# Kernel tuning notes

Measured on AMD Instinct MI355X. Metric: run time of the kernel, lower is better.

Reference implementation:

```python
import jax, jax.numpy as jnp
import numpy as np
from functools import partial


def lstm(x, Wx, Wh, b, act):
    """Keras LSTM. x:[B,T,F]. Gate order i,f,c,o. Returns (all_h:[B,T,H], last_h:[B,H])."""
    B, T, _ = x.shape
    H = Wh.shape[0]
    xz = jnp.einsum('btf,fg->btg', x, Wx) + b  # precompute input projections
    def step(carry, xz_t):
        h, c = carry
        z = xz_t + h @ Wh
        i, f, g, o = jnp.split(z, 4, axis=-1)
        i = jax.nn.sigmoid(i); f = jax.nn.sigmoid(f)
        g = act(g); o = jax.nn.sigmoid(o)
        c = f * c + i * g
        h = o * act(c)
        return (h, c), h
    init = (jnp.zeros((B, H), x.dtype), jnp.zeros((B, H), x.dtype))
    (h_last, _), hs = jax.lax.scan(step, init, jnp.swapaxes(xz, 0, 1))
    return jnp.swapaxes(hs, 0, 1), h_last


def gru(x, Wx, Wh, b):
    """Keras GRU with reset_after=True. b:[2,3H]. Gate order z,r,h. Returns last h."""
    B, T, _ = x.shape
    H = Wh.shape[0]
    xz = jnp.einsum('btf,fg->btg', x, Wx) + b[0]
    def step(h, xz_t):
        rec = h @ Wh + b[1]
        xz_z, xz_r, xz_h = jnp.split(xz_t, 3, axis=-1)
        r_z, r_r, r_h = jnp.split(rec, 3, axis=-1)
        z = jax.nn.sigmoid(xz_z + r_z)
        r = jax.nn.sigmoid(xz_r + r_r)
        hh = jnp.tanh(xz_h + r * r_h)
        h = z * h + (1.0 - z) * hh
        return h, None
    h0 = jnp.zeros((B, H), x.dtype)
    h_last, _ = jax.lax.scan(step, h0, jnp.swapaxes(xz, 0, 1))
    return h_last


def setup_inputs() -> dict:
    key = jax.random.key(0)
    ks = jax.random.split(key, 32)
    s = 0.05  # small init so relu-LSTM stays numerically stable over 64 steps
    d = {}
    d['keypoint_data'] = jax.random.normal(ks[0], (256, 64, 1662), jnp.float32)
    d['img_data'] = jax.random.normal(ks[1], (256, 64, 2048), jnp.float32)
    # keypoint LSTM stack: 1662->64->128->64, gates=4H
    d['kW1x'] = s * jax.random.normal(ks[2], (1662, 256), jnp.float32)
    d['kW1h'] = s * jax.random.normal(ks[3], (64, 256), jnp.float32)
    d['kb1'] = jnp.zeros((256,), jnp.float32)
    d['kW2x'] = s * jax.random.normal(ks[4], (64, 512), jnp.float32)
    d['kW2h'] = s * jax.random.normal(ks[5], (128, 512), jnp.float32)
    d['kb2'] = jnp.zeros((512,), jnp.float32)
    d['kW3x'] = s * jax.random.normal(ks[6], (128, 256), jnp.float32)
    d['kW3h'] = s * jax.random.normal(ks[7], (64, 256), jnp.float32)
    d['kb3'] = jnp.zeros((256,), jnp.float32)
    # keypoint dense heads
    d['kD1w'] = s * jax.random.normal(ks[8], (64, 64), jnp.float32)
    d['kD1b'] = jnp.zeros((64,), jnp.float32)
    d['kD2w'] = s * jax.random.normal(ks[9], (64, 32), jnp.float32)
    d['kD2b'] = jnp.zeros((32,), jnp.float32)
    # img branch: LSTM 2048->64 (tanh), GRU 64->8 (reset_after bias [2,24])
    d['iWx'] = s * jax.random.normal(ks[10], (2048, 256), jnp.float32)
    d['iWh'] = s * jax.random.normal(ks[11], (64, 256), jnp.float32)
    d['ib'] = jnp.zeros((256,), jnp.float32)
    d['gWx'] = s * jax.random.normal(ks[12], (64, 24), jnp.float32)
    d['gWh'] = s * jax.random.normal(ks[13], (8, 24), jnp.float32)
    d['gb'] = jnp.zeros((2, 24), jnp.float32)
    d['iDw'] = s * jax.random.normal(ks[14], (8, 8), jnp.float32)
    d['iDb'] = jnp.zeros((8,), jnp.float32)
    # final dense on concat([img(8), key(32)]) -> num_classes
    d['fW'] = s * jax.random.normal(ks[15], (40, 10), jnp.float32)
    d['fb'] = jnp.zeros((10,), jnp.float32)
    return d


def reference(keypoint_data, img_data,
              kW1x, kW1h, kb1, kW2x, kW2h, kb2, kW3x, kW3h, kb3,
              kD1w, kD1b, kD2w, kD2b,
              iWx, iWh, ib, gWx, gWh, gb, iDw, iDb, fW, fb):
    relu = jax.nn.relu
    # keypoint branch: 3 relu-LSTMs
    h, _ = lstm(keypoint_data, kW1x, kW1h, kb1, relu)
    h, _ = lstm(h, kW2x, kW2h, kb2, relu)
    _, h = lstm(h, kW3x, kW3h, kb3, relu)  # return_sequences=False
    h = relu(h @ kD1w + kD1b)
    key_out = relu(h @ kD2w + kD2b)  # [B,32]
    # img branch: tanh LSTM -> GRU -> (dropout=identity at inference) -> dense
    hs, _ = lstm(img_data, iWx, iWh, ib, jnp.tanh)
    g = gru(hs, gWx, gWh, gb)  # [B,8]
    img_out = relu(g @ iDw + iDb)  # [B,8]
    combined = jnp.concatenate([img_out, key_out], axis=-1)  # [B,40]
    return jax.nn.softmax(combined @ fW + fb, axis=-1)
```

## Files before the change

### kernel.cpp

```cpp
#include <hip/hip_runtime.h>


typedef short bf16x8 __attribute__((ext_vector_type(8)));
typedef float f32x4 __attribute__((ext_vector_type(4)));

__device__ __forceinline__ unsigned f2bf(float x) {
    unsigned u = __float_as_uint(x);
    return (u + 0x7FFFu + ((u >> 16) & 1u)) >> 16;
}
__device__ __forceinline__ float bf2f(unsigned b) { return __uint_as_float(b << 16); }
__device__ __forceinline__ float sigmoidf_(float x) { return 1.f / (1.f + __expf(-x)); }
__device__ __forceinline__ float tanhf_(float x) {
    float e = __expf(2.f * x);
    return 1.f - 2.f / (e + 1.f);
}

__device__ __forceinline__ void cvt2(float x0, float x1, unsigned& hp, unsigned& lp) {
    unsigned h;
    asm("v_cvt_pk_bf16_f32 %0, %1, %2" : "=v"(h) : "v"(x0), "v"(x1));
    float a0 = __uint_as_float(h << 16);
    float a1 = __uint_as_float(h & 0xffff0000u);
    unsigned l;
    asm("v_cvt_pk_bf16_f32 %0, %1, %2" : "=v"(l) : "v"(x0 - a0), "v"(x1 - a1));
    hp = h; lp = l;
}

template<int K, int N>
__device__ __forceinline__ void split_w(const float* __restrict__ W,
                                        unsigned short* __restrict__ hi,
                                        unsigned short* __restrict__ lo, int item) {
    int kt = item / N;
    int n  = item % N;
    unsigned uh[16], ul[16];
#pragma unroll
    for (int p = 0; p < 16; p++) {
        unsigned h2[2], l2[2];
#pragma unroll
        for (int e = 0; e < 2; e++) {
            int k = kt * 32 + p * 2 + e;
            float x = (k < K) ? W[(size_t)k * N + n] : 0.f;
            unsigned hb = f2bf(x);
            h2[e] = hb;
            l2[e] = f2bf(x - bf2f(hb));
        }
        uh[p] = h2[0] | (h2[1] << 16);
        ul[p] = l2[0] | (l2[1] << 16);
    }
    size_t off = (size_t)(kt * N + n) * 32;
    uint4* dh = (uint4*)(hi + off);
    uint4* dl = (uint4*)(lo + off);
#pragma unroll
    for (int c = 0; c < 4; c++) {
        uint4 v; v.x = uh[c*4]; v.y = uh[c*4+1]; v.z = uh[c*4+2]; v.w = uh[c*4+3];
        dh[c] = v;
        uint4 u; u.x = ul[c*4]; u.y = ul[c*4+1]; u.z = ul[c*4+2]; u.w = ul[c*4+3];
        dl[c] = u;
    }
}

__global__ __launch_bounds__(256) void split_all(
    const float* kW1x, const float* iWx, const float* kW2x, const float* kW3x,
    unsigned short* w1h, unsigned short* w1l, unsigned short* wih, unsigned short* wil,
    unsigned short* w2h, unsigned short* w2l, unsigned short* w3h, unsigned short* w3l) {
    int wid = blockIdx.x * 256 + threadIdx.x;
    if (wid < 13312)       split_w<1662, 256>(kW1x, w1h, w1l, wid);
    else if (wid < 29696)  split_w<2048, 256>(iWx,  wih, wil, wid - 13312);
    else if (wid < 30720)  split_w<64,   512>(kW2x, w2h, w2l, wid - 29696);
    else if (wid < 31744)  split_w<128,  256>(kW3x, w3h, w3l, wid - 30720);
}

__global__ __launch_bounds__(256, 2) void gemm_rd(
    const float* __restrict__ A, const unsigned short* __restrict__ Bhi,
    const unsigned short* __restrict__ Blo, const float* __restrict__ bias,
    float* __restrict__ out0, float* __restrict__ out1,
    int Kreal, int Kt, int Nfull) {
    const int m0  = blockIdx.x * 128;
    const int n0  = blockIdx.y * 128;
    const int ks  = blockIdx.z;
    const int nks = gridDim.z;
    const int ktChunk = Kt / nks;
    const int kt0 = ks * ktChunk;
    const int G   = ktChunk / 2;
    const int tid = threadIdx.x;
    const int lane = tid & 63;
    const int wv   = tid >> 6;
    const int l15  = lane & 15;
    const int q    = lane >> 4;
    const int row  = tid >> 1;
    const int kc   = tid & 1;

    __shared__ unsigned short Ah[2][2][128 * 40], Al[2][2][128 * 40];

    f32x4 acc[8][2];
#pragma unroll
    for (int i = 0; i < 8; i++)
#pragma unroll
        for (int j = 0; j < 2; j++) acc[i][j] = (f32x4){0.f, 0.f, 0.f, 0.f};

    auto loadA = [&](int g, float* r) {
        int kb = (kt0 + 2 * g + kc) * 32;
        const float* ap = A + (size_t)(m0 + row) * Kreal + kb;
        if (kb + 32 <= Kreal) {
#pragma unroll
            for (int j = 0; j < 16; j++) {
                float2 p = *(const float2*)(ap + 2 * j);
                r[2*j] = p.x; r[2*j+1] = p.y;
            }
        } else {
#pragma unroll
            for (int j = 0; j < 16; j++) {
                int gk = kb + 2 * j;
                r[2*j]   = (gk     < Kreal) ? ap[2*j]   : 0.f;
                r[2*j+1] = (gk + 1 < Kreal) ? ap[2*j+1] : 0.f;
            }
        }
    };
    auto writeA = [&](int buf, const float* r) {
        unsigned ph[16], pl[16];
#pragma unroll
        for (int p = 0; p < 16; p++) cvt2(r[2*p], r[2*p+1], ph[p], pl[p]);
        uint4* dh = (uint4*)&Ah[buf][kc][row * 40];
        uint4* dl = (uint4*)&Al[buf][kc][row * 40];
#pragma unroll
        for (int c = 0; c < 4; c++) {
            uint4 v; v.x = ph[c*4]; v.y = ph[c*4+1]; v.z = ph[c*4+2]; v.w = ph[c*4+3];
            dh[c] = v;
            uint4 u; u.x = pl[c*4]; u.y = pl[c*4+1]; u.z = pl[c*4+2]; u.w = pl[c*4+3];
            dl[c] = u;
        }
    };

    float r0[32];
    loadA(0, r0);
    writeA(0, r0);

    for (int g = 0; g < G; g++) {
        int buf = g & 1;
        __syncthreads();
        float rn[32];
        if (g + 1 < G) loadA(g + 1, rn);
#pragma unroll
        for (int sub = 0; sub < 2; sub++) {
            int ktg = kt0 + 2 * g + sub;
            bf16x8 bh[2], bl[2];
#pragma unroll
            for (int nt = 0; nt < 2; nt++) {
                size_t boff = ((size_t)ktg * Nfull + n0 + wv * 32 + nt * 16 + l15) * 32 + q * 8;
                bh[nt] = *(const bf16x8*)(Bhi + boff);
                bl[nt] = *(const bf16x8*)(Blo + boff);
            }
#pragma unroll
            for (int mt = 0; mt < 8; mt++) {
                int o = (mt * 16 + l15) * 40 + q * 8;
                bf16x8 ah = *(const bf16x8*)&Ah[buf][sub][o];
                bf16x8 al = *(const bf16x8*)&Al[buf][sub][o];
#pragma unroll
                for (int nt = 0; nt < 2; nt++) {
                    acc[mt][nt] = __builtin_amdgcn_mfma_f32_16x16x32_bf16(ah, bh[nt], acc[mt][nt], 0, 0, 0);
                    acc[mt][nt] = __builtin_amdgcn_mfma_f32_16x16x32_bf16(ah, bl[nt], acc[mt][nt], 0, 0, 0);
                    acc[mt][nt] = __builtin_amdgcn_mfma_f32_16x16x32_bf16(al, bh[nt], acc[mt][nt], 0, 0, 0);
                }
            }
        }
        if (g + 1 < G) writeA(buf ^ 1, rn);
    }
    float* op = (ks == 0) ? out0 : out1;
#pragma unroll
    for (int nt = 0; nt < 2; nt++) {
        int gcol = n0 + wv * 32 + nt * 16 + l15;
        float bv = (ks == 0) ? bias[gcol] : 0.f;
#pragma unroll
        for (int mt = 0; mt < 8; mt++)
#pragma unroll
            for (int r = 0; r < 4; r++) {
                int grow = m0 + mt * 16 + q * 4 + r;
                op[(size_t)grow * Nfull + gcol] = acc[mt][nt][r] + bv;
            }
    }
}

__global__ __launch_bounds__(256) void lstm_h64(
    int nA,
    const float* __restrict__ xA0, const float* __restrict__ xA1,
    const float* __restrict__ WhA, float* __restrict__ hA, int actA,
    const float* __restrict__ xB0, const float* __restrict__ xB1,
    const float* __restrict__ WhB, float* __restrict__ hB, int actB) {
    int bid = blockIdx.x;
    bool sec = bid >= nA;
    int b = sec ? bid - nA : bid;
    const float* x0 = sec ? xB0 : xA0;
    const float* x1 = sec ? xB1 : xA1;
    const float* Wh = sec ? WhB : WhA;
    float* hout     = sec ? hB  : hA;
    int act         = sec ? actB : actA;
    bool has1 = (x1 != nullptr);

    int g = threadIdx.x;
    float w[64];
#pragma unroll
    for (int k = 0; k < 64; k++) w[k] = Wh[k * 256 + g];

    __shared__ alignas(16) float hs[64];
    __shared__ float za[256];
    if (g < 64) hs[g] = 0.f;
    float c = 0.f;
    __syncthreads();

    const float* x0r = x0 + (size_t)b * 64 * 256;
    const float* x1r = has1 ? x1 + (size_t)b * 64 * 256 : x0r;
    float* hr = hout + (size_t)b * 64 * 64;
    bool isc = (g >= 128) && (g < 192);
    float cur = x0r[g] + (has1 ? x1r[g] : 0.f);
    for (int t = 0; t < 64; t++) {
        float nxt = 0.f;
        if (t < 63) {
            nxt = x0r[(t + 1) * 256 + g];
            if (has1) nxt += x1r[(t + 1) * 256 + g];
        }
        float z0 = cur, z1 = 0.f, z2 = 0.f, z3 = 0.f;
#pragma unroll
        for (int kk = 0; kk < 16; kk++) {
            float4 h4 = *(const float4*)&hs[kk * 4];
            z0 = fmaf(h4.x, w[kk * 4 + 0], z0);
            z1 = fmaf(h4.y, w[kk * 4 + 1], z1);
            z2 = fmaf(h4.z, w[kk * 4 + 2], z2);
            z3 = fmaf(h4.w, w[kk * 4 + 3], z3);
        }
        float z = (z0 + z1) + (z2 + z3);
        float a;
        if (isc) a = (act == 0) ? fmaxf(z, 0.f) : tanhf_(z);
        else     a = sigmoidf_(z);
        za[g] = a;
        __syncthreads();
        if (g < 64) {
            float iv = za[g], fv = za[64 + g], cd = za[128 + g], ov = za[192 + g];
            c = fmaf(fv, c, iv * cd);
            float ca = (act == 0) ? fmaxf(c, 0.f) : tanhf_(c);
            float h = ov * ca;
            hs[g] = h;
            hr[t * 64 + g] = h;
        }
        __syncthreads();
        cur = nxt;
    }
}

__global__ __launch_bounds__(512, 2) void lstm_h128(
    const float* __restrict__ xz, const float* __restrict__ Wh, float* __restrict__ hout) {
    int b = blockIdx.x;
    int g = threadIdx.x;
    float w[128];
#pragma unroll
    for (int k = 0; k < 128; k++) w[k] = Wh[k * 512 + g];

    __shared__ alignas(16) float hs[128];
    __shared__ float za[512];
    if (g < 128) hs[g] = 0.f;
    float c = 0.f;
    __syncthreads();

    const float* xzr = xz + (size_t)b * 64 * 512;
    float* hr = hout + (size_t)b * 64 * 128;
    bool isc = (g >= 256) && (g < 384);
    float cur = xzr[g];
    for (int t = 0; t < 64; t++) {
        float nxt = 0.f;
        if (t < 63) nxt = xzr[(t + 1) * 512 + g];
        float z0 = cur, z1 = 0.f, z2 = 0.f, z3 = 0.f;
#pragma unroll
        for (int kk = 0; kk < 32; kk++) {
            float4 h4 = *(const float4*)&hs[kk * 4];
            z0 = fmaf(h4.x, w[kk * 4 + 0], z0);
            z1 = fmaf(h4.y, w[kk * 4 + 1], z1);
            z2 = fmaf(h4.z, w[kk * 4 + 2], z2);
            z3 = fmaf(h4.w, w[kk * 4 + 3], z3);
        }
        float z = (z0 + z1) + (z2 + z3);
        float a = isc ? fmaxf(z, 0.f) : sigmoidf_(z);
        za[g] = a;
        __syncthreads();
        if (g < 128) {
            float iv = za[g], fv = za[128 + g], cd = za[256 + g], ov = za[384 + g];
            c = fmaf(fv, c, iv * cd);
            float h = ov * fmaxf(c, 0.f);
            hs[g] = h;
            hr[t * 128 + g] = h;
        }
        __syncthreads();
        cur = nxt;
    }
}

__global__ __launch_bounds__(64) void gru_kernel(
    const float* __restrict__ hsimg, const float* __restrict__ gWx,
    const float* __restrict__ gWh, const float* __restrict__ gb,
    float* __restrict__ glast) {
    int b = blockIdx.x;
    int qq = threadIdx.x;
    int col = (qq < 24) ? qq : 0;
    float wx[64], wh[8];
#pragma unroll
    for (int k = 0; k < 64; k++) wx[k] = gWx[k * 24 + col];
#pragma unroll
    for (int k = 0; k < 8; k++)  wh[k] = gWh[k * 24 + col];
    float b0 = gb[col], b1 = gb[24 + col];

    float hval = 0.f;
    const float* hb = hsimg + (size_t)b * 64 * 64;
    float cur = hb[qq];
    for (int t = 0; t < 64; t++) {
        float nxt = (t < 63) ? hb[(t + 1) * 64 + qq] : 0.f;
        float s0 = b0, s1 = 0.f, s2 = 0.f, s3 = 0.f;
#pragma unroll
        for (int k = 0; k < 64; k += 4) {
            s0 = fmaf(__shfl(cur, k + 0), wx[k + 0], s0);
            s1 = fmaf(__shfl(cur, k + 1), wx[k + 1], s1);
            s2 = fmaf(__shfl(cur, k + 2), wx[k + 2], s2);
            s3 = fmaf(__shfl(cur, k + 3), wx[k + 3], s3);
        }
        float sx = (s0 + s1) + (s2 + s3);
        float sr = b1;
#pragma unroll
        for (int k = 0; k < 8; k++) sr = fmaf(__shfl(hval, k), wh[k], sr);
        float xzz = __shfl(sx, qq),      rzz = __shfl(sr, qq);
        float xzr = __shfl(sx, 8 + qq),  rzr = __shfl(sr, 8 + qq);
        float xzh = __shfl(sx, 16 + qq), rzh = __shfl(sr, 16 + qq);
        float zz = sigmoidf_(xzz + rzz);
        float rv = sigmoidf_(xzr + rzr);
        float hc = tanhf_(xzh + rv * rzh);
        hval = zz * hval + (1.f - zz) * hc;
        cur = nxt;
    }
    if (qq < 8) glast[b * 8 + qq] = hval;
}

__global__ __launch_bounds__(64) void final_head(
    const float* __restrict__ h3seq, const float* __restrict__ glast,
    const float* __restrict__ kD1w, const float* __restrict__ kD1b,
    const float* __restrict__ kD2w, const float* __restrict__ kD2b,
    const float* __restrict__ iDw,  const float* __restrict__ iDb,
    const float* __restrict__ fW,   const float* __restrict__ fb,
    float* __restrict__ outp) {
    int b = blockIdx.x * 64 + threadIdx.x;
    float h3[64];
#pragma unroll
    for (int k = 0; k < 64; k++) h3[k] = h3seq[((size_t)b * 64 + 63) * 64 + k];
    float d1[64];
#pragma unroll
    for (int j = 0; j < 64; j++) {
        float s = kD1b[j];
#pragma unroll
        for (int k = 0; k < 64; k++) s = fmaf(h3[k], kD1w[k * 64 + j], s);
        d1[j] = fmaxf(s, 0.f);
    }
    float d2[32];
#pragma unroll
    for (int j = 0; j < 32; j++) {
        float s = kD2b[j];
#pragma unroll
        for (int k = 0; k < 64; k++) s = fmaf(d1[k], kD2w[k * 32 + j], s);
        d2[j] = fmaxf(s, 0.f);
    }
    float gi[8];
#pragma unroll
    for (int k = 0; k < 8; k++) gi[k] = glast[b * 8 + k];
    float io[8];
#pragma unroll
    for (int j = 0; j < 8; j++) {
        float s = iDb[j];
#pragma unroll
        for (int k = 0; k < 8; k++) s = fmaf(gi[k], iDw[k * 8 + j], s);
        io[j] = fmaxf(s, 0.f);
    }
    float lg[10];
#pragma unroll
    for (int j = 0; j < 10; j++) {
        float s = fb[j];
#pragma unroll
        for (int k = 0; k < 8; k++)  s = fmaf(io[k], fW[k * 10 + j], s);
#pragma unroll
        for (int k = 0; k < 32; k++) s = fmaf(d2[k], fW[(8 + k) * 10 + j], s);
        lg[j] = s;
    }
    float mx = lg[0];
#pragma unroll
    for (int j = 1; j < 10; j++) mx = fmaxf(mx, lg[j]);
    float den = 0.f, ex[10];
#pragma unroll
    for (int j = 0; j < 10; j++) { ex[j] = __expf(lg[j] - mx); den += ex[j]; }
    float inv = 1.f / den;
#pragma unroll
    for (int j = 0; j < 10; j++) outp[b * 10 + j] = ex[j] * inv;
}

extern "C" void kernel_launch(void* const* d_in, const int* in_sizes, int n_in,
                              void* d_out, int out_size, void* d_ws, size_t ws_size,
                              hipStream_t stream) {
    const float* keypoint = (const float*)d_in[0];
    const float* img      = (const float*)d_in[1];
    const float* kW1x = (const float*)d_in[2];
    const float* kW1h = (const float*)d_in[3];
    const float* kb1  = (const float*)d_in[4];
    const float* kW2x = (const float*)d_in[5];
    const float* kW2h = (const float*)d_in[6];
    const float* kb2  = (const float*)d_in[7];
    const float* kW3x = (const float*)d_in[8];
    const float* kW3h = (const float*)d_in[9];
    const float* kb3  = (const float*)d_in[10];
    const float* kD1w = (const float*)d_in[11];
    const float* kD1b = (const float*)d_in[12];
    const float* kD2w = (const float*)d_in[13];
    const float* kD2b = (const float*)d_in[14];
    const float* iWx  = (const float*)d_in[15];
    const float* iWh  = (const float*)d_in[16];
    const float* ib   = (const float*)d_in[17];
    const float* gWx  = (const float*)d_in[18];
    const float* gWh  = (const float*)d_in[19];
    const float* gb   = (const float*)d_in[20];
    const float* iDw  = (const float*)d_in[21];
    const float* iDb  = (const float*)d_in[22];
    const float* fW   = (const float*)d_in[23];
    const float* fb   = (const float*)d_in[24];
    float* outp = (float*)d_out;

    char* ws = (char*)d_ws;
    const size_t MB16 = (size_t)16384 * 256 * 4;
    float* r1a = (float*)(ws);
    float* r1b = (float*)(ws + MB16);
    float* r2a = (float*)(ws + 2 * MB16);
    float* r2b = (float*)(ws + 3 * MB16);
    size_t off = 4 * MB16;
    float* h1seq = (float*)(ws + off); off += (size_t)16384 * 64 * 4;
    float* h2seq = (float*)(ws + off); off += (size_t)16384 * 128 * 4;
    float* hsimg = (float*)(ws + off); off += (size_t)16384 * 64 * 4;
    float* glast = (float*)(ws + off); off += (size_t)256 * 8 * 4;
    unsigned short* w1h = (unsigned short*)(ws + off); off += (size_t)52 * 256 * 32 * 2;
    unsigned short* w1l = (unsigned short*)(ws + off); off += (size_t)52 * 256 * 32 * 2;
    unsigned short* wih = (unsigned short*)(ws + off); off += (size_t)64 * 256 * 32 * 2;
    unsigned short* wil = (unsigned short*)(ws + off); off += (size_t)64 * 256 * 32 * 2;
    unsigned short* w2h = (unsigned short*)(ws + off); off += (size_t)2 * 512 * 32 * 2;
    unsigned short* w2l = (unsigned short*)(ws + off); off += (size_t)2 * 512 * 32 * 2;
    unsigned short* w3h = (unsigned short*)(ws + off); off += (size_t)4 * 256 * 32 * 2;
    unsigned short* w3l = (unsigned short*)(ws + off); off += (size_t)4 * 256 * 32 * 2;
    float* xz2   = r2a;
    float* h3seq = h1seq;

    split_all<<<124, 256, 0, stream>>>(kW1x, iWx, kW2x, kW3x,
                                       w1h, w1l, wih, wil, w2h, w2l, w3h, w3l);
    gemm_rd<<<dim3(128, 2, 2), 256, 0, stream>>>(keypoint, w1h, w1l, kb1, r1a, r1b, 1662, 52, 256);
    gemm_rd<<<dim3(128, 2, 2), 256, 0, stream>>>(img, wih, wil, ib, r2a, r2b, 2048, 64, 256);
    lstm_h64<<<512, 256, 0, stream>>>(256, r1a, r1b, kW1h, h1seq, 0, r2a, r2b, iWh, hsimg, 1);
    gemm_rd<<<dim3(128, 4, 1), 256, 0, stream>>>(h1seq, w2h, w2l, kb2, xz2, xz2, 64, 2, 512);
    lstm_h128<<<256, 512, 0, stream>>>(xz2, kW2h, h2seq);
    gemm_rd<<<dim3(128, 2, 2), 256, 0, stream>>>(h2seq, w3h, w3l, kb3, r1a, r1b, 128, 4, 256);
    lstm_h64<<<256, 256, 0, stream>>>(256, r1a, r1b, kW3h, h3seq, 0, r1a, r1b, kW3h, h3seq, 0);
    gru_kernel<<<256, 64, 0, stream>>>(hsimg, gWx, gWh, gb, glast);
    final_head<<<4, 64, 0, stream>>>(h3seq, glast, kD1w, kD1b, kD2w, kD2b,
                                     iDw, iDb, fW, fb, outp);
    (void)in_sizes; (void)n_in; (void)out_size; (void)ws_size;
}
```

Before: 712.9 us.

## Software-pipeline B fragment and A global loads two stages ahead in GEMM

Restructures the gemm_rd main loop into a manually unrolled two-stage pipeline. B fragments for the next k-group and A data for the group after that are now fetched from global memory before the current MFMA work starts, with one barrier per stage. The aim is to hide global load latency behind MFMA compute. The cost is more live registers (two A staging buffers and two sets of B fragments), which may cut occupancy under launch_bounds(256,2). G is also changed to round up, which alters how odd k-tile chunks are counted.

```diff
diff --git a/kernel.cpp b/kernel.cpp
--- a/kernel.cpp
+++ b/kernel.cpp
@@ -80,7 +80,7 @@
     const int nks = gridDim.z;
     const int ktChunk = Kt / nks;
     const int kt0 = ks * ktChunk;
-    const int G   = ktChunk / 2;
+    const int G   = (ktChunk + 1) / 2;
     const int tid = threadIdx.x;
     const int lane = tid & 63;
     const int wv   = tid >> 6;
@@ -129,26 +129,19 @@
             dl[c] = u;
         }
     };
-
-    float r0[32];
-    loadA(0, r0);
-    writeA(0, r0);
-
-    for (int g = 0; g < G; g++) {
-        int buf = g & 1;
-        __syncthreads();
-        float rn[32];
-        if (g + 1 < G) loadA(g + 1, rn);
-#pragma unroll
-        for (int sub = 0; sub < 2; sub++) {
-            int ktg = kt0 + 2 * g + sub;
-            bf16x8 bh[2], bl[2];
+    auto loadB = [&](int g, bf16x8* bh, bf16x8* bl) {
+#pragma unroll
+        for (int sub = 0; sub < 2; sub++)
 #pragma unroll
             for (int nt = 0; nt < 2; nt++) {
-                size_t boff = ((size_t)ktg * Nfull + n0 + wv * 32 + nt * 16 + l15) * 32 + q * 8;
-                bh[nt] = *(const bf16x8*)(Bhi + boff);
-                bl[nt] = *(const bf16x8*)(Blo + boff);
+                size_t boff = ((size_t)(kt0 + 2 * g + sub) * Nfull + n0 + wv * 32 + nt * 16 + l15) * 32 + q * 8;
+                bh[sub * 2 + nt] = *(const bf16x8*)(Bhi + boff);
+                bl[sub * 2 + nt] = *(const bf16x8*)(Blo + boff);
             }
+    };
+    auto compute = [&](int buf, const bf16x8* bh, const bf16x8* bl) {
+#pragma unroll
+        for (int sub = 0; sub < 2; sub++)
 #pragma unroll
             for (int mt = 0; mt < 8; mt++) {
                 int o = (mt * 16 + l15) * 40 + q * 8;
@@ -156,14 +149,36 @@
                 bf16x8 al = *(const bf16x8*)&Al[buf][sub][o];
 #pragma unroll
                 for (int nt = 0; nt < 2; nt++) {
-                    acc[mt][nt] = __builtin_amdgcn_mfma_f32_16x16x32_bf16(ah, bh[nt], acc[mt][nt], 0, 0, 0);
-                    acc[mt][nt] = __builtin_amdgcn_mfma_f32_16x16x32_bf16(ah, bl[nt], acc[mt][nt], 0, 0, 0);
-                    acc[mt][nt] = __builtin_amdgcn_mfma_f32_16x16x32_bf16(al, bh[nt], acc[mt][nt], 0, 0, 0);
+                    acc[mt][nt] = __builtin_amdgcn_mfma_f32_16x16x32_bf16(ah, bh[sub*2+nt], acc[mt][nt], 0, 0, 0);
+                    acc[mt][nt] = __builtin_amdgcn_mfma_f32_16x16x32_bf16(ah, bl[sub*2+nt], acc[mt][nt], 0, 0, 0);
+                    acc[mt][nt] = __builtin_amdgcn_mfma_f32_16x16x32_bf16(al, bh[sub*2+nt], acc[mt][nt], 0, 0, 0);
                 }
             }
-        }
-        if (g + 1 < G) writeA(buf ^ 1, rn);
-    }
+    };
+
+    float  rA[32], rB[32];
+    bf16x8 bhA[4], blA[4], bhB[4], blB[4];
+    loadA(0, rA);
+    writeA(0, rA);
+    loadB(0, bhA, blA);
+    if (G > 1) loadA(1, rB);
+    __syncthreads();
+
+    for (int g = 0; g < G; g += 2) {
+        if (g + 1 < G) loadB(g + 1, bhB, blB);
+        if (g + 2 < G) loadA(g + 2, rA);
+        compute(0, bhA, blA);
+        if (g + 1 < G) writeA(1, rB);
+        __syncthreads();
+        if (g + 1 < G) {
+            if (g + 2 < G) loadB(g + 2, bhA, blA);
+            if (g + 3 < G) loadA(g + 3, rB);
+            compute(1, bhB, blB);
+            if (g + 2 < G) writeA(0, rA);
+            __syncthreads();
+        }
+    }
+
     float* op = (ks == 0) ? out0 : out1;
 #pragma unroll
     for (int nt = 0; nt < 2; nt++) {
```

After: 687.3 us. 3.6% less time.
